# Performance work log

Measured on AMD Instinct MI355X. Metric: run time of the kernel, lower is better.

The kernel has to match this reference:

```python
import jax, jax.numpy as jnp
import numpy as np

B, CIN, COUT = 16, 32, 64
T, H, W = 20, 32, 32
KT, KH, KW = 3, 3, 3
EPS = 1e-8
SURR_SCALE = 10.0  # SuperSpike surrogate slope


@jax.custom_vjp
def spike(x):
    # forward: heaviside; backward: SuperSpike surrogate gradient
    return (x > 0).astype(x.dtype)

def _spike_fwd(x):
    return (x > 0).astype(x.dtype), x

def _spike_bwd(x, g):
    return (g / (SURR_SCALE * jnp.abs(x) + 1.0) ** 2,)

spike.defvjp(_spike_fwd, _spike_bwd)


def _conv3d(x, w, pad, groups):
    return jax.lax.conv_general_dilated(
        x, w, window_strides=(1, 1, 1),
        padding=[(pad[0], pad[0]), (pad[1], pad[1]), (pad[2], pad[2])],
        rhs_dilation=(1, 1, 1),
        dimension_numbers=('NCDHW', 'OIDHW', 'NCDHW'),
        feature_group_count=groups)


def setup_inputs() -> dict:
    key = jax.random.key(0)
    k0, k1, k2 = jax.random.split(key, 3)
    w_init_mean, w_init_std = 0.05, 0.05
    w_mean = np.sqrt(w_init_mean)
    w_std = np.sqrt(np.sqrt(w_init_mean ** 2 + (w_init_std * np.sqrt(1.0 / (CIN * KT * KH * KW))) ** 2) - w_init_mean)
    x = jax.random.normal(k0, (B, CIN, T, H, W), dtype=jnp.float32)
    w_dw = w_mean + w_std * jax.random.normal(k1, (CIN, 1, KT, KH, KW), dtype=jnp.float32)
    w_pw = w_mean + w_std * jax.random.normal(k2, (COUT, CIN, 1, 1, 1), dtype=jnp.float32)
    beta = jnp.full((1,), 0.9, dtype=jnp.float32)  # one_per_layer, constant init, clamped [0,1]
    b = jnp.ones((COUT,), dtype=jnp.float32)       # constant init 1.0, clamped >= 0
    return {'x': x, 'w_dw': w_dw, 'w_pw': w_pw, 'beta': beta, 'b': b}


def reference(x, w_dw, w_pw, beta, b):
    pad = (1, 1, 1)  # ceil((3-1)*1/2) per dim; same padding also (faithfully) used for the 1x1x1 conv
    conv_x = _conv3d(x, w_dw, pad, CIN)[:, :, :, :H, :W]          # depthwise, crop to input_shape
    conv_x = _conv3d(conv_x, w_pw, pad, 1)[:, :, :, :H, :W]        # pointwise (time grows T -> T+2)
    nb_steps = conv_x.shape[2]

    # effective full kernel = depthwise * pointwise (broadcast over kernel dims)
    w_tmp = jnp.broadcast_to(jnp.transpose(w_dw, (1, 0, 2, 3, 4)), (COUT, CIN, KT, KH, KW)) * w_pw
    d = jnp.einsum('abcde,fbcde->af', w_tmp, w_tmp)                # lateral inhibition matrix [COUT, COUT]
    norm = (w_tmp ** 2).sum((1, 2, 3, 4))                          # [COUT]
    inv_norm = 1.0 / (norm + EPS)

    def step(carry, inp):
        mem, spk = carry
        rst = jnp.einsum('abcd,be->aecd', spk, d)                  # lateral reset
        mem = (mem - rst) * beta + inp * (1.0 - beta)              # leaky soft-reset update
        mthr = mem * inv_norm[None, :, None, None] - b[None, :, None, None]
        spk = spike(mthr)
        return (mem, spk), spk

    conv_t = jnp.moveaxis(conv_x, 2, 0)                            # [nb_steps, B, COUT, H, W]
    zeros = jnp.zeros((B, COUT, H, W), dtype=x.dtype)
    _, spks = jax.lax.scan(step, (zeros, zeros), conv_t)
    spk_rec = jnp.moveaxis(spks, 0, 2)                             # [B, COUT, nb_steps, H, W]

    loss = 0.5 * (spk_rec ** 2).mean()                             # 'squared'
    spk_spread_loss = spk_rec.sum((0, 1, 3, 4)).max() / (B * COUT * H * W)  # 'max'
    return spk_rec, loss, spk_spread_loss
```

## Files before the change

### kernel.cpp

```cpp
#include <hip/hip_runtime.h>

#define BB_   16
#define CIN_  32
#define COUT_ 64
#define TT_   20
#define NSTEP 22
#define NPIX  1024
#define HW_   32

typedef float f32x16 __attribute__((ext_vector_type(16)));

#define N_DWOUT 10485760ULL
#define N_DW2   10485760ULL
#define OFF_DWOUT 0ULL
#define OFF_DW2   (OFF_DWOUT + N_DWOUT)
#define OFF_D     (OFF_DW2 + N_DW2)
#define OFF_INVN  (OFF_D + 4096ULL)
#define OFF_CNT   (OFF_INVN + 64ULL)
#define WS_FLOATS (OFF_CNT + 32ULL)

__global__ __launch_bounds__(128)
void k_depthwise(const float* __restrict__ x, const float* __restrict__ wdw,
                 float* __restrict__ dwout) {
    const int blk = blockIdx.x;
    const int t4 = blk & 3;
    const int ci = (blk >> 2) & 31;
    const int b  = blk >> 7;
    const int tid = threadIdx.x;
    __shared__ float pl[3][34][35];

    float w[27];
#pragma unroll
    for (int k = 0; k < 27; ++k) w[k] = wdw[ci * 27 + k];

    for (int i = tid; i < 3 * 34 * 35; i += 128) (&pl[0][0][0])[i] = 0.f;
    __syncthreads();

    const float* xb = x + (size_t)(b * 32 + ci) * TT_ * NPIX;
    const int lr = tid >> 2;
    const int lc = (tid & 3) * 8;

    auto load_plane = [&](int p, int slot) {
        const float* s = xb + (size_t)p * NPIX + lr * 32 + lc;
        float4 v0 = *(const float4*)s;
        float4 v1 = *(const float4*)(s + 4);
        float* d = &pl[slot][1 + lr][1 + lc];
        d[0] = v0.x; d[1] = v0.y; d[2] = v0.z; d[3] = v0.w;
        d[4] = v1.x; d[5] = v1.y; d[6] = v1.z; d[7] = v1.w;
    };
    auto zero_plane = [&](int slot) {
        float* d = &pl[slot][1 + lr][1 + lc];
#pragma unroll
        for (int j = 0; j < 8; ++j) d[j] = 0.f;
    };

    const int T0 = t4 * 5;
    if (T0 > 0) load_plane(T0 - 1, (T0 - 1) % 3);
    load_plane(T0, T0 % 3);

    const int hd = lr, wd0 = lc;
    const float* base = &pl[0][0][0];

    for (int t = T0; t < T0 + 5; ++t) {
        __syncthreads();
        const int pnext = t + 1;
        if (pnext < TT_) load_plane(pnext, pnext % 3);
        else             zero_plane(pnext % 3);
        __syncthreads();

        const int sm1 = (t + 2) % 3, s0 = t % 3, sp1 = (t + 1) % 3;
        float acc[8] = {0.f,0.f,0.f,0.f,0.f,0.f,0.f,0.f};
#pragma unroll
        for (int kt = 0; kt < 3; ++kt) {
            const int slot = (kt == 0) ? sm1 : (kt == 1) ? s0 : sp1;
            const float* Pp = base + slot * (34 * 35);
#pragma unroll
            for (int kh = 0; kh < 3; ++kh) {
                const float* row = Pp + (hd + kh) * 35 + wd0;
                float r[10];
#pragma unroll
                for (int m = 0; m < 10; ++m) r[m] = row[m];
#pragma unroll
                for (int kw = 0; kw < 3; ++kw) {
                    const float wv = w[(kt * 3 + kh) * 3 + kw];
#pragma unroll
                    for (int j = 0; j < 8; ++j) acc[j] = fmaf(wv, r[j + kw], acc[j]);
                }
            }
        }
        float* dst = dwout + ((size_t)(b * 32 + ci) * TT_ + t) * NPIX + hd * 32 + wd0;
        *(float4*)dst       = make_float4(acc[0], acc[1], acc[2], acc[3]);
        *(float4*)(dst + 4) = make_float4(acc[4], acc[5], acc[6], acc[7]);
    }
}

__global__ __launch_bounds__(256)
void k_dmat(const float* __restrict__ wdw, const float* __restrict__ wpw,
            float* __restrict__ dmat, float* __restrict__ invn,
            unsigned* __restrict__ gcnt) {
    __shared__ double S[32];
    const int tid = threadIdx.x;
    if (tid < NSTEP) gcnt[tid] = 0u;
    if (tid < 32) {
        double s = 0.0;
        for (int k = 0; k < 27; ++k) { double v = (double)wdw[tid * 27 + k]; s += v * v; }
        S[tid] = s;
    }
    __syncthreads();
    for (int e = tid; e < 4096; e += 256) {
        const int a = e >> 6, f = e & 63;
        double acc = 0.0;
        for (int ci = 0; ci < 32; ++ci)
            acc += (double)wpw[a * 32 + ci] * (double)wpw[f * 32 + ci] * S[ci];
        dmat[e] = (float)acc;
        if (a == f) invn[a] = (float)(1.0 / (acc + 1e-8));
    }
}

__global__ __launch_bounds__(256)
void k_transpose(const float* __restrict__ dwout, float* __restrict__ dw2) {
    const int blk = blockIdx.x;
    const int hq = blk & 7;
    const int bt = blk >> 3;
    const int t  = bt % 20;
    const int b  = bt / 20;
    const int tid = threadIdx.x;
    __shared__ float lt[32][33];
    const int wsrc = tid & 31, cg = tid >> 5;

    for (int hh = 0; hh < 4; ++hh) {
        const int h = hq * 4 + hh;
#pragma unroll
        for (int cc = 0; cc < 4; ++cc) {
            const int ci = cc * 8 + cg;
            lt[wsrc][ci] = dwout[((size_t)(b * 32 + ci) * TT_ + t) * NPIX + h * 32 + wsrc];
        }
        __syncthreads();
        float* drow = dw2 + ((size_t)(b * TT_ + t) * 32 + h) * NPIX;
#pragma unroll
        for (int ss = 0; ss < 4; ++ss) {
            const int slot = ss * 8 + cg;
            drow[slot * 32 + wsrc] = (slot == 0) ? 0.f : lt[slot - 1][wsrc];
        }
        __syncthreads();
    }
}

__global__ __launch_bounds__(512)
void k_recur(const float* __restrict__ dw2, const float* __restrict__ wpw,
             const float* __restrict__ dmat, const float* __restrict__ invn_g,
             const float* __restrict__ beta_g, const float* __restrict__ bvec,
             float* __restrict__ out, unsigned* __restrict__ gcnt) {
    const int blk = blockIdx.x;
    const int whalf = blk & 1;
    const int h = (blk >> 1) & 31;
    const int b = blk >> 6;
    const int tid = threadIdx.x;
    const int lane = tid & 63;
    const int co = lane;
    const int wid = __builtin_amdgcn_readfirstlane(tid >> 6);
    const int w0 = whalf * 16 + wid * 2;

    __shared__ float d_lds[4096];
    __shared__ unsigned long long msk[NSTEP][16];

    for (int i = tid; i < 4096; i += 512) d_lds[i] = dmat[i];
    {
        unsigned long long* mp = &msk[0][0];
        for (int i = tid; i < NSTEP * 16; i += 512) mp[i] = 0ull;
    }

    const float beta_v = beta_g[0];
    const float omb = 1.0f - beta_v;
    const float invn = invn_g[co];
    const float bth  = bvec[co];

    float wa[32];
#pragma unroll
    for (int ci = 0; ci < 32; ++ci) wa[ci] = wpw[co * 32 + ci];

    float mem0 = 0.f, mem1 = 0.f;
    unsigned long long m0p = 0ull, m1p = 0ull;

    {
        const int zco = tid >> 3, zw = (tid & 7) * 2;
        *(float2*)(out + ((size_t)(b * 64 + zco) * NSTEP) * NPIX + h * 32 + whalf * 16 + zw)
            = make_float2(0.f, 0.f);
    }

    __syncthreads();

    const int base0 = ((b * TT_) * 32 + (h - 1)) * NPIX + w0 * 32;
    const bool hok = (h >= 1);

    f32x16 A0, A1, A2, A3;
    if (hok) {
        const float* wrow = dw2 + (size_t)base0;
        A0 = *(const f32x16*)(wrow);
        A1 = *(const f32x16*)(wrow + 16);
        A2 = *(const f32x16*)(wrow + 32);
        A3 = *(const f32x16*)(wrow + 48);
    }

    for (int t = 1; t < NSTEP; ++t) {
        float inp0 = 0.f, inp1 = 0.f;
        if (hok && t <= TT_) {
#pragma unroll
            for (int ci = 0; ci < 16; ++ci) {
                inp0 = fmaf(wa[ci], A0[ci], inp0);
                inp1 = fmaf(wa[ci], A2[ci], inp1);
            }
#pragma unroll
            for (int ci = 0; ci < 16; ++ci) {
                inp0 = fmaf(wa[16 + ci], A1[ci], inp0);
                inp1 = fmaf(wa[16 + ci], A3[ci], inp1);
            }
        }
        if (hok && t < TT_) {
            const float* wrow = dw2 + (size_t)base0 + (size_t)t * (32 * NPIX);
            A0 = *(const f32x16*)(wrow);
            A1 = *(const f32x16*)(wrow + 16);
            A2 = *(const f32x16*)(wrow + 32);
            A3 = *(const f32x16*)(wrow + 48);
        }

        float rst0 = 0.f, rst1 = 0.f;
        unsigned long long mm = m0p;
        while (mm) { const int a = __builtin_ctzll(mm); mm &= mm - 1; rst0 += d_lds[a * 64 + co]; }
        mm = m1p;
        while (mm) { const int a = __builtin_ctzll(mm); mm &= mm - 1; rst1 += d_lds[a * 64 + co]; }

        const float u0 = (mem0 - rst0) * beta_v;
        mem0 = u0 + inp0 * omb;
        const bool s0 = (mem0 * invn - bth) > 0.f;
        const float u1 = (mem1 - rst1) * beta_v;
        mem1 = u1 + inp1 * omb;
        const bool s1 = (mem1 * invn - bth) > 0.f;

        m0p = __ballot(s0);
        m1p = __ballot(s1);
        const int wl = wid * 2;
        if (lane == 0) { msk[t][wl] = m0p; msk[t][wl + 1] = m1p; }
    }
    __syncthreads();

    if (tid < NSTEP) {
        unsigned c = 0;
        for (int w = 0; w < 16; ++w) c += (unsigned)__popcll(msk[tid][w]);
        if (c) atomicAdd(&gcnt[tid], c);
    }

    const int wl = tid & 15;
    for (int it = 0; it < 44; ++it) {
        const int r = it * 32 + (tid >> 4);
        const int tt = r >> 6, cc = r & 63;
        const unsigned long long wv = msk[tt][wl];
        const float sv = (float)((wv >> cc) & 1ull);
        out[((size_t)(b * 64 + cc) * NSTEP + tt) * NPIX + h * 32 + whalf * 16 + wl] = sv;
    }
}

__global__ void k_final(const unsigned* __restrict__ gcnt, float* __restrict__ out,
                        int out_size) {
    if (threadIdx.x == 0 && blockIdx.x == 0) {
        unsigned long long tot = 0; unsigned mx = 0;
        for (int t = 0; t < NSTEP; ++t) { const unsigned c = gcnt[t]; tot += c; if (c > mx) mx = c; }
        const long long nspk = (long long)out_size - 2;
        out[out_size - 2] = (float)(0.5 * ((double)tot / (double)nspk));
        out[out_size - 1] = (float)((double)mx / 1048576.0);
    }
}

extern "C" void kernel_launch(void* const* d_in, const int* in_sizes, int n_in,
                              void* d_out, int out_size, void* d_ws, size_t ws_size,
                              hipStream_t stream) {
    const float* x    = (const float*)d_in[0];
    const float* wdw  = (const float*)d_in[1];
    const float* wpw  = (const float*)d_in[2];
    const float* beta = (const float*)d_in[3];
    const float* bvec = (const float*)d_in[4];
    float* out = (float*)d_out;
    float* ws  = (float*)d_ws;

    if (ws_size < WS_FLOATS * sizeof(float)) return;

    float* dwout = ws + OFF_DWOUT;
    float* dw2   = ws + OFF_DW2;
    float* dmat  = ws + OFF_D;
    float* invn  = ws + OFF_INVN;
    unsigned* gcnt = (unsigned*)(ws + OFF_CNT);

    k_dmat     <<<1, 256, 0, stream>>>(wdw, wpw, dmat, invn, gcnt);
    k_depthwise<<<BB_ * CIN_ * 4, 128, 0, stream>>>(x, wdw, dwout);
    k_transpose<<<BB_ * TT_ * 8, 256, 0, stream>>>(dwout, dw2);
    k_recur    <<<BB_ * HW_ * 2, 512, 0, stream>>>(dw2, wpw, dmat, invn, beta, bvec, out, gcnt);
    k_final    <<<1, 64, 0, stream>>>(gcnt, out, out_size);
}
```

Baseline: 89.72 us.

## Fold dmat into depthwise launch and stream spike stores inside recurrence loop

```diff
diff --git a/kernel.cpp b/kernel.cpp
--- a/kernel.cpp
+++ b/kernel.cpp
@@ -19,14 +19,39 @@
 #define OFF_CNT   (OFF_INVN + 64ULL)
 #define WS_FLOATS (OFF_CNT + 32ULL)
 
+#define DW_BLOCKS (BB_ * CIN_ * 4)
+
 __global__ __launch_bounds__(128)
 void k_depthwise(const float* __restrict__ x, const float* __restrict__ wdw,
-                 float* __restrict__ dwout) {
+                 const float* __restrict__ wpw, float* __restrict__ dwout,
+                 float* __restrict__ dmat, float* __restrict__ invn,
+                 unsigned* __restrict__ gcnt) {
     const int blk = blockIdx.x;
+    const int tid = threadIdx.x;
+
+    if (blk == DW_BLOCKS) {
+        __shared__ double S[32];
+        if (tid < NSTEP) gcnt[tid] = 0u;
+        if (tid < 32) {
+            double s = 0.0;
+            for (int k = 0; k < 27; ++k) { double v = (double)wdw[tid * 27 + k]; s += v * v; }
+            S[tid] = s;
+        }
+        __syncthreads();
+        for (int e = tid; e < 4096; e += 128) {
+            const int a = e >> 6, f = e & 63;
+            double acc = 0.0;
+            for (int ci = 0; ci < 32; ++ci)
+                acc += (double)wpw[a * 32 + ci] * (double)wpw[f * 32 + ci] * S[ci];
+            dmat[e] = (float)acc;
+            if (a == f) invn[a] = (float)(1.0 / (acc + 1e-8));
+        }
+        return;
+    }
+
     const int t4 = blk & 3;
     const int ci = (blk >> 2) & 31;
     const int b  = blk >> 7;
-    const int tid = threadIdx.x;
     __shared__ float pl[3][34][35];
 
     float w[27];
@@ -91,29 +116,6 @@
         float* dst = dwout + ((size_t)(b * 32 + ci) * TT_ + t) * NPIX + hd * 32 + wd0;
         *(float4*)dst       = make_float4(acc[0], acc[1], acc[2], acc[3]);
         *(float4*)(dst + 4) = make_float4(acc[4], acc[5], acc[6], acc[7]);
-    }
-}
-
-__global__ __launch_bounds__(256)
-void k_dmat(const float* __restrict__ wdw, const float* __restrict__ wpw,
-            float* __restrict__ dmat, float* __restrict__ invn,
-            unsigned* __restrict__ gcnt) {
-    __shared__ double S[32];
-    const int tid = threadIdx.x;
-    if (tid < NSTEP) gcnt[tid] = 0u;
-    if (tid < 32) {
-        double s = 0.0;
-        for (int k = 0; k < 27; ++k) { double v = (double)wdw[tid * 27 + k]; s += v * v; }
-        S[tid] = s;
-    }
-    __syncthreads();
-    for (int e = tid; e < 4096; e += 256) {
-        const int a = e >> 6, f = e & 63;
-        double acc = 0.0;
-        for (int ci = 0; ci < 32; ++ci)
-            acc += (double)wpw[a * 32 + ci] * (double)wpw[f * 32 + ci] * S[ci];
-        dmat[e] = (float)acc;
-        if (a == f) invn[a] = (float)(1.0 / (acc + 1e-8));
     }
 }
 
@@ -182,13 +184,9 @@
     float mem0 = 0.f, mem1 = 0.f;
     unsigned long long m0p = 0ull, m1p = 0ull;
 
-    {
-        const int zco = tid >> 3, zw = (tid & 7) * 2;
-        *(float2*)(out + ((size_t)(b * 64 + zco) * NSTEP) * NPIX + h * 32 + whalf * 16 + zw)
-            = make_float2(0.f, 0.f);
-    }
-
-    __syncthreads();
+    const int scc = wid * 8 + (lane >> 3);
+    const int sws = (lane & 7) * 2;
+    const size_t sbase = ((size_t)(b * 64 + scc) * NSTEP) * NPIX + h * 32 + whalf * 16 + sws;
 
     const int base0 = ((b * TT_) * 32 + (h - 1)) * NPIX + w0 * 32;
     const bool hok = (h >= 1);
@@ -202,24 +200,39 @@
         A3 = *(const f32x16*)(wrow + 48);
     }
 
+    __syncthreads();
+
     for (int t = 1; t < NSTEP; ++t) {
+        {
+            const unsigned long long mA = msk[t - 1][sws];
+            const unsigned long long mB = msk[t - 1][sws + 1];
+            const float2 sv = make_float2((float)((mA >> scc) & 1ull),
+                                          (float)((mB >> scc) & 1ull));
+            *(float2*)(out + sbase + (size_t)(t - 1) * NPIX) = sv;
+        }
+
         float inp0 = 0.f, inp1 = 0.f;
-        if (hok && t <= TT_) {
-#pragma unroll
-            for (int ci = 0; ci < 16; ++ci) {
-                inp0 = fmaf(wa[ci], A0[ci], inp0);
-                inp1 = fmaf(wa[ci], A2[ci], inp1);
-            }
-#pragma unroll
-            for (int ci = 0; ci < 16; ++ci) {
-                inp0 = fmaf(wa[16 + ci], A1[ci], inp0);
-                inp1 = fmaf(wa[16 + ci], A3[ci], inp1);
-            }
-        }
-        if (hok && t < TT_) {
+        const bool gemm = hok && (t <= TT_);
+        const bool pf   = hok && (t < TT_);
+        if (gemm) {
+#pragma unroll
+            for (int ci = 0; ci < 16; ++ci) inp0 = fmaf(wa[ci], A0[ci], inp0);
+#pragma unroll
+            for (int ci = 0; ci < 16; ++ci) inp0 = fmaf(wa[16 + ci], A1[ci], inp0);
+        }
+        if (pf) {
             const float* wrow = dw2 + (size_t)base0 + (size_t)t * (32 * NPIX);
             A0 = *(const f32x16*)(wrow);
             A1 = *(const f32x16*)(wrow + 16);
+        }
+        if (gemm) {
+#pragma unroll
+            for (int ci = 0; ci < 16; ++ci) inp1 = fmaf(wa[ci], A2[ci], inp1);
+#pragma unroll
+            for (int ci = 0; ci < 16; ++ci) inp1 = fmaf(wa[16 + ci], A3[ci], inp1);
+        }
+        if (pf) {
+            const float* wrow = dw2 + (size_t)base0 + (size_t)t * (32 * NPIX);
             A2 = *(const f32x16*)(wrow + 32);
             A3 = *(const f32x16*)(wrow + 48);
         }
@@ -241,22 +254,22 @@
         m1p = __ballot(s1);
         const int wl = wid * 2;
         if (lane == 0) { msk[t][wl] = m0p; msk[t][wl + 1] = m1p; }
-    }
-    __syncthreads();
+
+        __syncthreads();
+    }
+
+    {
+        const unsigned long long mA = msk[NSTEP - 1][sws];
+        const unsigned long long mB = msk[NSTEP - 1][sws + 1];
+        const float2 sv = make_float2((float)((mA >> scc) & 1ull),
+                                      (float)((mB >> scc) & 1ull));
+        *(float2*)(out + sbase + (size_t)(NSTEP - 1) * NPIX) = sv;
+    }
 
     if (tid < NSTEP) {
         unsigned c = 0;
         for (int w = 0; w < 16; ++w) c += (unsigned)__popcll(msk[tid][w]);
         if (c) atomicAdd(&gcnt[tid], c);
-    }
-
-    const int wl = tid & 15;
-    for (int it = 0; it < 44; ++it) {
-        const int r = it * 32 + (tid >> 4);
-        const int tt = r >> 6, cc = r & 63;
-        const unsigned long long wv = msk[tt][wl];
-        const float sv = (float)((wv >> cc) & 1ull);
-        out[((size_t)(b * 64 + cc) * NSTEP + tt) * NPIX + h * 32 + whalf * 16 + wl] = sv;
     }
 }
 
@@ -290,8 +303,7 @@
     float* invn  = ws + OFF_INVN;
     unsigned* gcnt = (unsigned*)(ws + OFF_CNT);
 
-    k_dmat     <<<1, 256, 0, stream>>>(wdw, wpw, dmat, invn, gcnt);
-    k_depthwise<<<BB_ * CIN_ * 4, 128, 0, stream>>>(x, wdw, dwout);
+    k_depthwise<<<DW_BLOCKS + 1, 128, 0, stream>>>(x, wdw, wpw, dwout, dmat, invn, gcnt);
     k_transpose<<<BB_ * TT_ * 8, 256, 0, stream>>>(dwout, dw2);
     k_recur    <<<BB_ * HW_ * 2, 512, 0, stream>>>(dw2, wpw, dmat, invn, beta, bvec, out, gcnt);
     k_final    <<<1, 64, 0, stream>>>(gcnt, out, out_size);
```

New measurement: 100.5 us. 1.12x slower.

## Fold dmat into depthwise launch and move spike expansion to separate kernel

Applied to the files above, without the earlier changes.

```diff
diff --git a/kernel.cpp b/kernel.cpp
--- a/kernel.cpp
+++ b/kernel.cpp
@@ -17,16 +17,43 @@
 #define OFF_D     (OFF_DW2 + N_DW2)
 #define OFF_INVN  (OFF_D + 4096ULL)
 #define OFF_CNT   (OFF_INVN + 64ULL)
-#define WS_FLOATS (OFF_CNT + 32ULL)
+#define OFF_MSKG  (OFF_CNT + 32ULL)
+#define N_MSKG_F  (512ULL * NSTEP * 32ULL * 2ULL)
+#define WS_FLOATS (OFF_MSKG + N_MSKG_F)
+
+#define DW_BLOCKS (BB_ * CIN_ * 4)
 
 __global__ __launch_bounds__(128)
 void k_depthwise(const float* __restrict__ x, const float* __restrict__ wdw,
-                 float* __restrict__ dwout) {
+                 const float* __restrict__ wpw, float* __restrict__ dwout,
+                 float* __restrict__ dmat, float* __restrict__ invn,
+                 unsigned* __restrict__ gcnt) {
     const int blk = blockIdx.x;
+    const int tid = threadIdx.x;
+
+    if (blk == DW_BLOCKS) {
+        __shared__ double S[32];
+        if (tid < NSTEP) gcnt[tid] = 0u;
+        if (tid < 32) {
+            double s = 0.0;
+            for (int k = 0; k < 27; ++k) { double v = (double)wdw[tid * 27 + k]; s += v * v; }
+            S[tid] = s;
+        }
+        __syncthreads();
+        for (int e = tid; e < 4096; e += 128) {
+            const int a = e >> 6, f = e & 63;
+            double acc = 0.0;
+            for (int ci = 0; ci < 32; ++ci)
+                acc += (double)wpw[a * 32 + ci] * (double)wpw[f * 32 + ci] * S[ci];
+            dmat[e] = (float)acc;
+            if (a == f) invn[a] = (float)(1.0 / (acc + 1e-8));
+        }
+        return;
+    }
+
     const int t4 = blk & 3;
     const int ci = (blk >> 2) & 31;
     const int b  = blk >> 7;
-    const int tid = threadIdx.x;
     __shared__ float pl[3][34][35];
 
     float w[27];
@@ -95,29 +122,6 @@
 }
 
 __global__ __launch_bounds__(256)
-void k_dmat(const float* __restrict__ wdw, const float* __restrict__ wpw,
-            float* __restrict__ dmat, float* __restrict__ invn,
-            unsigned* __restrict__ gcnt) {
-    __shared__ double S[32];
-    const int tid = threadIdx.x;
-    if (tid < NSTEP) gcnt[tid] = 0u;
-    if (tid < 32) {
-        double s = 0.0;
-        for (int k = 0; k < 27; ++k) { double v = (double)wdw[tid * 27 + k]; s += v * v; }
-        S[tid] = s;
-    }
-    __syncthreads();
-    for (int e = tid; e < 4096; e += 256) {
-        const int a = e >> 6, f = e & 63;
-        double acc = 0.0;
-        for (int ci = 0; ci < 32; ++ci)
-            acc += (double)wpw[a * 32 + ci] * (double)wpw[f * 32 + ci] * S[ci];
-        dmat[e] = (float)acc;
-        if (a == f) invn[a] = (float)(1.0 / (acc + 1e-8));
-    }
-}
-
-__global__ __launch_bounds__(256)
 void k_transpose(const float* __restrict__ dwout, float* __restrict__ dw2) {
     const int blk = blockIdx.x;
     const int hq = blk & 7;
@@ -150,7 +154,7 @@
 void k_recur(const float* __restrict__ dw2, const float* __restrict__ wpw,
              const float* __restrict__ dmat, const float* __restrict__ invn_g,
              const float* __restrict__ beta_g, const float* __restrict__ bvec,
-             float* __restrict__ out, unsigned* __restrict__ gcnt) {
+             unsigned long long* __restrict__ mskg, unsigned* __restrict__ gcnt) {
     const int blk = blockIdx.x;
     const int whalf = blk & 1;
     const int h = (blk >> 1) & 31;
@@ -165,10 +169,6 @@
     __shared__ unsigned long long msk[NSTEP][16];
 
     for (int i = tid; i < 4096; i += 512) d_lds[i] = dmat[i];
-    {
-        unsigned long long* mp = &msk[0][0];
-        for (int i = tid; i < NSTEP * 16; i += 512) mp[i] = 0ull;
-    }
 
     const float beta_v = beta_g[0];
     const float omb = 1.0f - beta_v;
@@ -181,14 +181,6 @@
 
     float mem0 = 0.f, mem1 = 0.f;
     unsigned long long m0p = 0ull, m1p = 0ull;
-
-    {
-        const int zco = tid >> 3, zw = (tid & 7) * 2;
-        *(float2*)(out + ((size_t)(b * 64 + zco) * NSTEP) * NPIX + h * 32 + whalf * 16 + zw)
-            = make_float2(0.f, 0.f);
-    }
-
-    __syncthreads();
 
     const int base0 = ((b * TT_) * 32 + (h - 1)) * NPIX + w0 * 32;
     const bool hok = (h >= 1);
@@ -202,6 +194,8 @@
         A3 = *(const f32x16*)(wrow + 48);
     }
 
+    __syncthreads();
+
     for (int t = 1; t < NSTEP; ++t) {
         float inp0 = 0.f, inp1 = 0.f;
         if (hok && t <= TT_) {
@@ -244,19 +238,45 @@
     }
     __syncthreads();
 
-    if (tid < NSTEP) {
+    if (tid < NSTEP * 16) {
+        const int t = tid >> 4, wl = tid & 15;
+        const size_t row = (size_t)((b * 32 + h) * NSTEP + t);
+        mskg[row * 32 + whalf * 16 + wl] = (t == 0) ? 0ull : msk[t][wl];
+    }
+
+    if (tid >= 1 && tid < NSTEP) {
         unsigned c = 0;
         for (int w = 0; w < 16; ++w) c += (unsigned)__popcll(msk[tid][w]);
         if (c) atomicAdd(&gcnt[tid], c);
     }
-
-    const int wl = tid & 15;
-    for (int it = 0; it < 44; ++it) {
-        const int r = it * 32 + (tid >> 4);
-        const int tt = r >> 6, cc = r & 63;
-        const unsigned long long wv = msk[tt][wl];
-        const float sv = (float)((wv >> cc) & 1ull);
-        out[((size_t)(b * 64 + cc) * NSTEP + tt) * NPIX + h * 32 + whalf * 16 + wl] = sv;
+}
+
+__global__ __launch_bounds__(256)
+void k_expand(const unsigned long long* __restrict__ mskg, float* __restrict__ out) {
+    const int b = blockIdx.x >> 5, h = blockIdx.x & 31;
+    const int tid = threadIdx.x;
+    __shared__ unsigned long long lm[NSTEP * 32];
+    const size_t mbase = (size_t)(b * 32 + h) * NSTEP * 32;
+    for (int i = tid; i < NSTEP * 32; i += 256) lm[i] = mskg[mbase + i];
+    __syncthreads();
+
+    const int co = tid >> 2, wq = tid & 3;
+    float* obase = out + (size_t)(b * 64 + co) * NSTEP * NPIX + h * 32 + wq * 8;
+#pragma unroll 2
+    for (int t = 0; t < NSTEP; ++t) {
+        const unsigned long long* mr = &lm[t * 32 + wq * 8];
+        float4 o0, o1;
+        o0.x = (float)((mr[0] >> co) & 1ull);
+        o0.y = (float)((mr[1] >> co) & 1ull);
+        o0.z = (float)((mr[2] >> co) & 1ull);
+        o0.w = (float)((mr[3] >> co) & 1ull);
+        o1.x = (float)((mr[4] >> co) & 1ull);
+        o1.y = (float)((mr[5] >> co) & 1ull);
+        o1.z = (float)((mr[6] >> co) & 1ull);
+        o1.w = (float)((mr[7] >> co) & 1ull);
+        float* dst = obase + (size_t)t * NPIX;
+        *(float4*)dst       = o0;
+        *(float4*)(dst + 4) = o1;
     }
 }
 
@@ -289,10 +309,11 @@
     float* dmat  = ws + OFF_D;
     float* invn  = ws + OFF_INVN;
     unsigned* gcnt = (unsigned*)(ws + OFF_CNT);
-
-    k_dmat     <<<1, 256, 0, stream>>>(wdw, wpw, dmat, invn, gcnt);
-    k_depthwise<<<BB_ * CIN_ * 4, 128, 0, stream>>>(x, wdw, dwout);
+    unsigned long long* mskg = (unsigned long long*)(ws + OFF_MSKG);
+
+    k_depthwise<<<DW_BLOCKS + 1, 128, 0, stream>>>(x, wdw, wpw, dwout, dmat, invn, gcnt);
     k_transpose<<<BB_ * TT_ * 8, 256, 0, stream>>>(dwout, dw2);
-    k_recur    <<<BB_ * HW_ * 2, 512, 0, stream>>>(dw2, wpw, dmat, invn, beta, bvec, out, gcnt);
+    k_recur    <<<BB_ * HW_ * 2, 512, 0, stream>>>(dw2, wpw, dmat, invn, beta, bvec, mskg, gcnt);
+    k_expand   <<<BB_ * HW_, 256, 0, stream>>>(mskg, out);
     k_final    <<<1, 64, 0, stream>>>(gcnt, out, out_size);
 }
```

Result: slower. 113.9 us (+26.9%).

## Fuse depthwise conv, transpose and dmat setup into one kernel

Applied to the files above, without the earlier changes.

```diff
diff --git a/kernel.cpp b/kernel.cpp
--- a/kernel.cpp
+++ b/kernel.cpp
@@ -10,140 +10,124 @@
 
 typedef float f32x16 __attribute__((ext_vector_type(16)));
 
-#define N_DWOUT 10485760ULL
 #define N_DW2   10485760ULL
-#define OFF_DWOUT 0ULL
-#define OFF_DW2   (OFF_DWOUT + N_DWOUT)
+#define OFF_DW2   0ULL
 #define OFF_D     (OFF_DW2 + N_DW2)
 #define OFF_INVN  (OFF_D + 4096ULL)
 #define OFF_CNT   (OFF_INVN + 64ULL)
 #define WS_FLOATS (OFF_CNT + 32ULL)
 
-__global__ __launch_bounds__(128)
-void k_depthwise(const float* __restrict__ x, const float* __restrict__ wdw,
-                 float* __restrict__ dwout) {
+#define DWT_BLOCKS (BB_ * TT_ * 8)
+
+__global__ __launch_bounds__(256)
+void k_dwt(const float* __restrict__ x, const float* __restrict__ wdw,
+           const float* __restrict__ wpw, float* __restrict__ dw2,
+           float* __restrict__ dmat, float* __restrict__ invn,
+           unsigned* __restrict__ gcnt) {
     const int blk = blockIdx.x;
-    const int t4 = blk & 3;
-    const int ci = (blk >> 2) & 31;
-    const int b  = blk >> 7;
     const int tid = threadIdx.x;
-    __shared__ float pl[3][34][35];
-
-    float w[27];
-#pragma unroll
-    for (int k = 0; k < 27; ++k) w[k] = wdw[ci * 27 + k];
-
-    for (int i = tid; i < 3 * 34 * 35; i += 128) (&pl[0][0][0])[i] = 0.f;
-    __syncthreads();
-
-    const float* xb = x + (size_t)(b * 32 + ci) * TT_ * NPIX;
-    const int lr = tid >> 2;
-    const int lc = (tid & 3) * 8;
-
-    auto load_plane = [&](int p, int slot) {
-        const float* s = xb + (size_t)p * NPIX + lr * 32 + lc;
-        float4 v0 = *(const float4*)s;
-        float4 v1 = *(const float4*)(s + 4);
-        float* d = &pl[slot][1 + lr][1 + lc];
-        d[0] = v0.x; d[1] = v0.y; d[2] = v0.z; d[3] = v0.w;
-        d[4] = v1.x; d[5] = v1.y; d[6] = v1.z; d[7] = v1.w;
-    };
-    auto zero_plane = [&](int slot) {
-        float* d = &pl[slot][1 + lr][1 + lc];
-#pragma unroll
-        for (int j = 0; j < 8; ++j) d[j] = 0.f;
-    };
-
-    const int T0 = t4 * 5;
-    if (T0 > 0) load_plane(T0 - 1, (T0 - 1) % 3);
-    load_plane(T0, T0 % 3);
-
-    const int hd = lr, wd0 = lc;
-    const float* base = &pl[0][0][0];
-
-    for (int t = T0; t < T0 + 5; ++t) {
+
+    if (blk == DWT_BLOCKS) {
+        __shared__ double S[32];
+        if (tid < NSTEP) gcnt[tid] = 0u;
+        if (tid < 32) {
+            double s = 0.0;
+            for (int k = 0; k < 27; ++k) { double v = (double)wdw[tid * 27 + k]; s += v * v; }
+            S[tid] = s;
+        }
         __syncthreads();
-        const int pnext = t + 1;
-        if (pnext < TT_) load_plane(pnext, pnext % 3);
-        else             zero_plane(pnext % 3);
-        __syncthreads();
-
-        const int sm1 = (t + 2) % 3, s0 = t % 3, sp1 = (t + 1) % 3;
-        float acc[8] = {0.f,0.f,0.f,0.f,0.f,0.f,0.f,0.f};
-#pragma unroll
-        for (int kt = 0; kt < 3; ++kt) {
-            const int slot = (kt == 0) ? sm1 : (kt == 1) ? s0 : sp1;
-            const float* Pp = base + slot * (34 * 35);
-#pragma unroll
-            for (int kh = 0; kh < 3; ++kh) {
-                const float* row = Pp + (hd + kh) * 35 + wd0;
-                float r[10];
-#pragma unroll
-                for (int m = 0; m < 10; ++m) r[m] = row[m];
-#pragma unroll
-                for (int kw = 0; kw < 3; ++kw) {
-                    const float wv = w[(kt * 3 + kh) * 3 + kw];
-#pragma unroll
-                    for (int j = 0; j < 8; ++j) acc[j] = fmaf(wv, r[j + kw], acc[j]);
-                }
-            }
-        }
-        float* dst = dwout + ((size_t)(b * 32 + ci) * TT_ + t) * NPIX + hd * 32 + wd0;
-        *(float4*)dst       = make_float4(acc[0], acc[1], acc[2], acc[3]);
-        *(float4*)(dst + 4) = make_float4(acc[4], acc[5], acc[6], acc[7]);
-    }
-}
-
-__global__ __launch_bounds__(256)
-void k_dmat(const float* __restrict__ wdw, const float* __restrict__ wpw,
-            float* __restrict__ dmat, float* __restrict__ invn,
-            unsigned* __restrict__ gcnt) {
-    __shared__ double S[32];
-    const int tid = threadIdx.x;
-    if (tid < NSTEP) gcnt[tid] = 0u;
-    if (tid < 32) {
-        double s = 0.0;
-        for (int k = 0; k < 27; ++k) { double v = (double)wdw[tid * 27 + k]; s += v * v; }
-        S[tid] = s;
-    }
-    __syncthreads();
-    for (int e = tid; e < 4096; e += 256) {
-        const int a = e >> 6, f = e & 63;
-        double acc = 0.0;
-        for (int ci = 0; ci < 32; ++ci)
-            acc += (double)wpw[a * 32 + ci] * (double)wpw[f * 32 + ci] * S[ci];
-        dmat[e] = (float)acc;
-        if (a == f) invn[a] = (float)(1.0 / (acc + 1e-8));
-    }
-}
-
-__global__ __launch_bounds__(256)
-void k_transpose(const float* __restrict__ dwout, float* __restrict__ dw2) {
-    const int blk = blockIdx.x;
+        for (int e = tid; e < 4096; e += 256) {
+            const int a = e >> 6, f = e & 63;
+            double acc = 0.0;
+            for (int ci = 0; ci < 32; ++ci)
+                acc += (double)wpw[a * 32 + ci] * (double)wpw[f * 32 + ci] * S[ci];
+            dmat[e] = (float)acc;
+            if (a == f) invn[a] = (float)(1.0 / (acc + 1e-8));
+        }
+        return;
+    }
+
     const int hq = blk & 7;
     const int bt = blk >> 3;
-    const int t  = bt % 20;
-    const int b  = bt / 20;
-    const int tid = threadIdx.x;
-    __shared__ float lt[32][33];
-    const int wsrc = tid & 31, cg = tid >> 5;
-
-    for (int hh = 0; hh < 4; ++hh) {
-        const int h = hq * 4 + hh;
-#pragma unroll
-        for (int cc = 0; cc < 4; ++cc) {
-            const int ci = cc * 8 + cg;
-            lt[wsrc][ci] = dwout[((size_t)(b * 32 + ci) * TT_ + t) * NPIX + h * 32 + wsrc];
-        }
-        __syncthreads();
-        float* drow = dw2 + ((size_t)(b * TT_ + t) * 32 + h) * NPIX;
-#pragma unroll
-        for (int ss = 0; ss < 4; ++ss) {
-            const int slot = ss * 8 + cg;
-            drow[slot * 32 + wsrc] = (slot == 0) ? 0.f : lt[slot - 1][wsrc];
-        }
-        __syncthreads();
-    }
+    const int t  = bt % TT_;
+    const int b  = bt / TT_;
+    const int h0 = hq * 4;
+
+    __shared__ float xl[3][32][6][35];
+    float* xp = &xl[0][0][0][0];
+
+    for (int i = tid; i < 3 * 32 * 6 * 35; i += 256) xp[i] = 0.f;
+    __syncthreads();
+
+    for (int i = tid; i < 3 * 32 * 6 * 8; i += 256) {
+        const int f4  = i & 7;
+        const int row = i >> 3;
+        const int r   = row % 6;
+        const int ci  = (row / 6) & 31;
+        const int k   = row / 192;
+        const int tt  = t - 1 + k;
+        const int hh  = h0 - 1 + r;
+        if (tt >= 0 && tt < TT_ && hh >= 0 && hh < 32) {
+            const float4 v = *(const float4*)(x + ((size_t)(b * 32 + ci) * TT_ + tt) * NPIX + hh * 32 + f4 * 4);
+            float* d = &xl[k][ci][r][1 + f4 * 4];
+            d[0] = v.x; d[1] = v.y; d[2] = v.z; d[3] = v.w;
+        }
+    }
+    __syncthreads();
+
+    const int ci = tid >> 3;
+    const int sub = tid & 7;
+    const int lh = sub >> 1;
+    const int wh = sub & 1;
+    const int w0 = wh * 16;
+
+    float wreg[27];
+#pragma unroll
+    for (int k = 0; k < 27; ++k) wreg[k] = wdw[ci * 27 + k];
+
+    float acc[16];
+#pragma unroll
+    for (int j = 0; j < 16; ++j) acc[j] = 0.f;
+
+#pragma unroll
+    for (int kt = 0; kt < 3; ++kt) {
+#pragma unroll
+        for (int kh = 0; kh < 3; ++kh) {
+            const float* row = &xl[kt][ci][lh + kh][w0];
+            float r[18];
+#pragma unroll
+            for (int m = 0; m < 18; ++m) r[m] = row[m];
+#pragma unroll
+            for (int kw = 0; kw < 3; ++kw) {
+                const float wv = wreg[(kt * 3 + kh) * 3 + kw];
+#pragma unroll
+                for (int j = 0; j < 16; ++j) acc[j] = fmaf(wv, r[j + kw], acc[j]);
+            }
+        }
+    }
+    __syncthreads();
+
+#pragma unroll
+    for (int j = 0; j < 16; ++j) xp[(lh * 32 + w0 + j) * 33 + ci] = acc[j];
+    __syncthreads();
+
+    const int lh2 = tid >> 6;
+    const int wp  = (tid & 63) * 16;
+    const int slot = wp >> 5;
+    const int ci0  = wp & 31;
+    float4 o[4];
+    if (slot == 0) {
+#pragma unroll
+        for (int q = 0; q < 4; ++q) o[q] = make_float4(0.f, 0.f, 0.f, 0.f);
+    } else {
+        const float* src = &xp[(lh2 * 32 + (slot - 1)) * 33 + ci0];
+#pragma unroll
+        for (int q = 0; q < 4; ++q)
+            o[q] = make_float4(src[q * 4], src[q * 4 + 1], src[q * 4 + 2], src[q * 4 + 3]);
+    }
+    float* dst = dw2 + ((size_t)(b * TT_ + t) * 32 + h0 + lh2) * NPIX + slot * 32 + ci0;
+#pragma unroll
+    for (int q = 0; q < 4; ++q) *(float4*)(dst + q * 4) = o[q];
 }
 
 __global__ __launch_bounds__(512)
@@ -284,15 +268,12 @@
 
     if (ws_size < WS_FLOATS * sizeof(float)) return;
 
-    float* dwout = ws + OFF_DWOUT;
     float* dw2   = ws + OFF_DW2;
     float* dmat  = ws + OFF_D;
     float* invn  = ws + OFF_INVN;
     unsigned* gcnt = (unsigned*)(ws + OFF_CNT);
 
-    k_dmat     <<<1, 256, 0, stream>>>(wdw, wpw, dmat, invn, gcnt);
-    k_depthwise<<<BB_ * CIN_ * 4, 128, 0, stream>>>(x, wdw, dwout);
-    k_transpose<<<BB_ * TT_ * 8, 256, 0, stream>>>(dwout, dw2);
-    k_recur    <<<BB_ * HW_ * 2, 512, 0, stream>>>(dw2, wpw, dmat, invn, beta, bvec, out, gcnt);
-    k_final    <<<1, 64, 0, stream>>>(gcnt, out, out_size);
-}
+    k_dwt  <<<DWT_BLOCKS + 1, 256, 0, stream>>>(x, wdw, wpw, dw2, dmat, invn, gcnt);
+    k_recur<<<BB_ * HW_ * 2, 512, 0, stream>>>(dw2, wpw, dmat, invn, beta, bvec, out, gcnt);
+    k_final<<<1, 64, 0, stream>>>(gcnt, out, out_size);
+}
```

Result: slower. 150.0 us (+67.2%).
